# Performance work log

Measured on AMD Instinct MI355X. Metric: run time of the kernel, lower is better.

## Reference

```python
import jax, jax.numpy as jnp
import numpy as np


def sobel_kernels_3d(dtype=jnp.float32):
    # Standard 3D Sobel: derivative [-1,0,1] along one axis, smoothing [1,2,1]
    # along the other two. Returns shape (3, 1, 3, 3, 3) in OIDHW layout.
    s = jnp.array([1.0, 2.0, 1.0], dtype=dtype)
    d = jnp.array([-1.0, 0.0, 1.0], dtype=dtype)
    kd = jnp.einsum('i,j,k->ijk', d, s, s)  # d/dD
    kh = jnp.einsum('i,j,k->ijk', s, d, s)  # d/dH
    kw = jnp.einsum('i,j,k->ijk', s, s, d)  # d/dW
    return jnp.stack([kd, kh, kw], axis=0)[:, None]  # (3,1,3,3,3)


def _grad3d(x, kernels):
    # x: (B, C, D, H, W) -> flatten (B*C, 1, D, H, W), conv with padding=1.
    B, C, D, H, W = x.shape
    x_ = x.reshape(B * C, 1, D, H, W)
    return jax.lax.conv_general_dilated(
        x_, kernels.astype(x.dtype),
        window_strides=(1, 1, 1),
        padding=((1, 1), (1, 1), (1, 1)),
        dimension_numbers=('NCDHW', 'OIDHW', 'NCDHW'),
    )  # (B*C, 3, D, H, W)


def setup_inputs() -> dict:
    key = jax.random.key(0)
    k1, k2 = jax.random.split(key)
    shape = (4, 4, 64, 128, 128)
    pred = jax.random.normal(k1, shape, dtype=jnp.float32)
    target = jax.random.normal(k2, shape, dtype=jnp.float32)
    return {"pred": pred, "target": target}


def reference(pred, target):
    kernels = sobel_kernels_3d(pred.dtype)
    grad_pred = _grad3d(pred, kernels)
    grad_target = _grad3d(target, kernels)
    # loss_type == 'l1'
    return jnp.mean(jnp.abs(grad_pred - grad_target))
```

## Files before the change

kernel.cpp:

```cpp
#include <hip/hip_runtime.h>

#define NB 16
#define DD 64
#define HH 128
#define WW 128
#define HW (HH * WW)

constexpr int CD = 2;
constexpr int TH = 8;
constexpr int LZ = CD + 2;
constexpr int LY = TH + 2;
constexpr int PL = LY * WW;
constexpr int NPOS = LZ * LY * (WW / 4);
constexpr int SLOTS = NPOS / 256;
constexpr int NT = 8;
constexpr int NQ = 4;
constexpr float INV_COUNT = 1.0f / 50331648.0f;

__global__ void zero_out_kernel(float* out) {
    if (threadIdx.x == 0 && blockIdx.x == 0) out[0] = 0.0f;
}

__global__ __launch_bounds__(256) void sobel_l1_kernel(
    const float* __restrict__ pred,
    const float* __restrict__ target,
    float* __restrict__ out)
{
    __shared__ float t[2][LZ * PL];

    const int tid = threadIdx.x;
    int b = blockIdx.x;
    const int bh   = b & 15; b >>= 4;
    const int q    = b & 3;  b >>= 2;
    const int bn   = b;

    const int h0 = bh * TH;
    const int dbase = q * (NT * CD);
    const size_t nbase = (size_t)bn * (size_t)(DD * HW);

    int  soff[SLOTS];
    int  sz[SLOTS];
    bool sokh[SLOTS];
#pragma unroll
    for (int k = 0; k < SLOTS; ++k) {
        const int i  = k * 256 + tid;
        const int q4 = i & 31;
        const int ry = i >> 5;
        const int z  = ry / LY;
        const int y  = ry - z * LY;
        const int gh = h0 - 1 + y;
        sokh[k] = (unsigned)gh < HH;
        soff[k] = min(max(gh, 0), HH - 1) * WW + 4 * q4;
        sz[k]   = z;
    }

    float4 sp[SLOTS], sq[SLOTS];

    auto load_tile = [&](int tau) {
        const int d0 = dbase + tau * CD;
#pragma unroll
        for (int k = 0; k < SLOTS; ++k) {
            const int gd  = d0 - 1 + sz[k];
            const int gdc = min(max(gd, 0), DD - 1);
            const size_t idx = nbase + (size_t)gdc * HW + soff[k];
            sp[k] = *(const float4*)(pred + idx);
            sq[k] = *(const float4*)(target + idx);
        }
    };

    auto store_tile = [&](int tau, float* B) {
        const int d0 = dbase + tau * CD;
#pragma unroll
        for (int k = 0; k < SLOTS; ++k) {
            const int gd = d0 - 1 + sz[k];
            const float m = (sokh[k] && (unsigned)gd < DD) ? 1.0f : 0.0f;
            const int i = k * 256 + tid;
            const float4 v = float4{(sp[k].x - sq[k].x) * m,
                                    (sp[k].y - sq[k].y) * m,
                                    (sp[k].z - sq[k].z) * m,
                                    (sp[k].w - sq[k].w) * m};
            *(float4*)&B[4 * i] = v;
        }
    };

    const int tc = tid & 31;
    const int lh = tid >> 5;

    auto compute_tile = [&](const float* B, float& acc) {
        auto plane_l = [&](int z, float4& A_, float4& Bh_, float4& Bw_) {
            float4 rs[3], rdw[3];
#pragma unroll
            for (int r = 0; r < 3; ++r) {
                const float4 v = *(const float4*)&B[z * PL + (lh + r) * WW + 4 * tc];
                float lm = __shfl_up(v.w, 1, 32);
                float rp = __shfl_down(v.x, 1, 32);
                if (tc == 0)  lm = 0.f;
                if (tc == 31) rp = 0.f;
                rs[r]  = float4{lm  + 2.f * v.x + v.y,
                                v.x + 2.f * v.y + v.z,
                                v.y + 2.f * v.z + v.w,
                                v.z + 2.f * v.w + rp};
                rdw[r] = float4{v.y - lm, v.z - v.x, v.w - v.y, rp - v.z};
            }
            A_  = float4{rs[0].x + 2.f * rs[1].x + rs[2].x,
                         rs[0].y + 2.f * rs[1].y + rs[2].y,
                         rs[0].z + 2.f * rs[1].z + rs[2].z,
                         rs[0].w + 2.f * rs[1].w + rs[2].w};
            Bh_ = float4{rs[2].x - rs[0].x, rs[2].y - rs[0].y,
                         rs[2].z - rs[0].z, rs[2].w - rs[0].w};
            Bw_ = float4{rdw[0].x + 2.f * rdw[1].x + rdw[2].x,
                         rdw[0].y + 2.f * rdw[1].y + rdw[2].y,
                         rdw[0].z + 2.f * rdw[1].z + rdw[2].z,
                         rdw[0].w + 2.f * rdw[1].w + rdw[2].w};
        };

        float4 rA[3], rBh[3], rBw[3];
        plane_l(0, rA[0], rBh[0], rBw[0]);
        plane_l(1, rA[1], rBh[1], rBw[1]);
#pragma unroll
        for (int ld = 0; ld < CD; ++ld) {
            const int s0 = ld % 3, s1 = (ld + 1) % 3, s2 = (ld + 2) % 3;
            plane_l(ld + 2, rA[s2], rBh[s2], rBw[s2]);
            const float4 a0 = rA[s0],  a2 = rA[s2];
            const float4 b0 = rBh[s0], b1 = rBh[s1], b2 = rBh[s2];
            const float4 c0 = rBw[s0], c1 = rBw[s1], c2 = rBw[s2];
            acc += fabsf(a2.x - a0.x) + fabsf(a2.y - a0.y)
                 + fabsf(a2.z - a0.z) + fabsf(a2.w - a0.w);
            acc += fabsf(b0.x + 2.f * b1.x + b2.x) + fabsf(b0.y + 2.f * b1.y + b2.y)
                 + fabsf(b0.z + 2.f * b1.z + b2.z) + fabsf(b0.w + 2.f * b1.w + b2.w);
            acc += fabsf(c0.x + 2.f * c1.x + c2.x) + fabsf(c0.y + 2.f * c1.y + c2.y)
                 + fabsf(c0.z + 2.f * c1.z + c2.z) + fabsf(c0.w + 2.f * c1.w + c2.w);
        }
    };

    float acc = 0.0f;
    load_tile(0);
    store_tile(0, t[0]);
    __syncthreads();
    for (int tau = 0; tau < NT; ++tau) {
        if (tau + 1 < NT) load_tile(tau + 1);
        compute_tile(t[tau & 1], acc);
        if (tau + 1 < NT) store_tile(tau + 1, t[(tau + 1) & 1]);
        __syncthreads();
    }

#pragma unroll
    for (int off = 32; off > 0; off >>= 1)
        acc += __shfl_down(acc, off, 64);
    if ((tid & 63) == 0) t[0][tid >> 6] = acc;
    __syncthreads();
    if (tid == 0) {
        const float s = t[0][0] + t[0][1] + t[0][2] + t[0][3];
        atomicAdd(out, s * INV_COUNT);
    }
}

extern "C" void kernel_launch(void* const* d_in, const int* in_sizes, int n_in,
                              void* d_out, int out_size, void* d_ws, size_t ws_size,
                              hipStream_t stream) {
    const float* pred   = (const float*)d_in[0];
    const float* target = (const float*)d_in[1];
    float* out = (float*)d_out;

    zero_out_kernel<<<1, 64, 0, stream>>>(out);

    const int nblocks = NB * NQ * (HH / TH);
    sobel_l1_kernel<<<nblocks, 256, 0, stream>>>(pred, target, out);
}
```

Before: 155.4 us.

## Replace double-buffered depth tiles with a six-plane LDS ring buffer

Each depth step previously loaded four planes from global memory into a fresh shared-memory buffer, re-reading the two halo planes the previous step already held. This version keeps a six-plane ring in shared memory and fetches only the two new planes per step, with the remaining 128-thread slot handling the plane remainder. The goal is to roughly halve global read traffic and cut LDS usage, which, together with a launch-bounds occupancy hint, could allow more resident blocks. The cost is extra indexing and ring-slot arithmetic, plus an uneven load split across threads.

```diff
diff --git a/kernel.cpp b/kernel.cpp
--- a/kernel.cpp
+++ b/kernel.cpp
@@ -6,92 +6,96 @@
 #define WW 128
 #define HW (HH * WW)
 
-constexpr int CD = 2;
 constexpr int TH = 8;
-constexpr int LZ = CD + 2;
 constexpr int LY = TH + 2;
 constexpr int PL = LY * WW;
-constexpr int NPOS = LZ * LY * (WW / 4);
-constexpr int SLOTS = NPOS / 256;
+constexpr int RING = 6;
 constexpr int NT = 8;
 constexpr int NQ = 4;
+constexpr int SLOTS = 3;
 constexpr float INV_COUNT = 1.0f / 50331648.0f;
 
 __global__ void zero_out_kernel(float* out) {
     if (threadIdx.x == 0 && blockIdx.x == 0) out[0] = 0.0f;
 }
 
-__global__ __launch_bounds__(256) void sobel_l1_kernel(
+__global__ __launch_bounds__(256, 4) void sobel_l1_kernel(
     const float* __restrict__ pred,
     const float* __restrict__ target,
     float* __restrict__ out)
 {
-    __shared__ float t[2][LZ * PL];
+    __shared__ float ring[RING * PL];
 
     const int tid = threadIdx.x;
     int b = blockIdx.x;
-    const int bh   = b & 15; b >>= 4;
-    const int q    = b & 3;  b >>= 2;
-    const int bn   = b;
+    const int bh = b & 15; b >>= 4;
+    const int q  = b & 3;  b >>= 2;
+    const int bn = b;
 
     const int h0 = bh * TH;
-    const int dbase = q * (NT * CD);
+    const int dbase = q * (NT * 2);
     const size_t nbase = (size_t)bn * (size_t)(DD * HW);
 
+    const bool k2ok = tid < 128;
     int  soff[SLOTS];
+    int  stoff[SLOTS];
     int  sz[SLOTS];
     bool sokh[SLOTS];
 #pragma unroll
     for (int k = 0; k < SLOTS; ++k) {
-        const int i  = k * 256 + tid;
-        const int q4 = i & 31;
-        const int ry = i >> 5;
-        const int z  = ry / LY;
-        const int y  = ry - z * LY;
+        const int i  = (k < 2) ? (k * 256 + tid) : (512 + (tid & 127));
+        const int z  = i / 320;
+        const int r  = i - z * 320;
+        const int y  = r >> 5;
+        const int q4 = r & 31;
         const int gh = h0 - 1 + y;
-        sokh[k] = (unsigned)gh < HH;
-        soff[k] = min(max(gh, 0), HH - 1) * WW + 4 * q4;
-        sz[k]   = z;
+        sokh[k]  = (unsigned)gh < HH;
+        soff[k]  = min(max(gh, 0), HH - 1) * WW + 4 * q4;
+        stoff[k] = y * WW + 4 * q4;
+        sz[k]    = z;
     }
 
     float4 sp[SLOTS], sq[SLOTS];
 
-    auto load_tile = [&](int tau) {
-        const int d0 = dbase + tau * CD;
+    auto load_pair = [&](int p0) {
 #pragma unroll
         for (int k = 0; k < SLOTS; ++k) {
-            const int gd  = d0 - 1 + sz[k];
-            const int gdc = min(max(gd, 0), DD - 1);
-            const size_t idx = nbase + (size_t)gdc * HW + soff[k];
-            sp[k] = *(const float4*)(pred + idx);
-            sq[k] = *(const float4*)(target + idx);
+            if (k < 2 || k2ok) {
+                const int gd  = dbase + p0 + sz[k];
+                const int gdc = min(max(gd, 0), DD - 1);
+                const size_t idx = nbase + (size_t)gdc * HW + soff[k];
+                sp[k] = *(const float4*)(pred + idx);
+                sq[k] = *(const float4*)(target + idx);
+            }
         }
     };
 
-    auto store_tile = [&](int tau, float* B) {
-        const int d0 = dbase + tau * CD;
+    auto store_pair = [&](int p0) {
+        const int base0 = ((p0 + 1) % RING) * PL;
+        const int base1 = ((p0 + 2) % RING) * PL;
 #pragma unroll
         for (int k = 0; k < SLOTS; ++k) {
-            const int gd = d0 - 1 + sz[k];
-            const float m = (sokh[k] && (unsigned)gd < DD) ? 1.0f : 0.0f;
-            const int i = k * 256 + tid;
-            const float4 v = float4{(sp[k].x - sq[k].x) * m,
-                                    (sp[k].y - sq[k].y) * m,
-                                    (sp[k].z - sq[k].z) * m,
-                                    (sp[k].w - sq[k].w) * m};
-            *(float4*)&B[4 * i] = v;
+            if (k < 2 || k2ok) {
+                const int gd = dbase + p0 + sz[k];
+                const float m = (sokh[k] && (unsigned)gd < DD) ? 1.0f : 0.0f;
+                float* dst = &ring[(sz[k] ? base1 : base0) + stoff[k]];
+                *(float4*)dst = float4{(sp[k].x - sq[k].x) * m,
+                                       (sp[k].y - sq[k].y) * m,
+                                       (sp[k].z - sq[k].z) * m,
+                                       (sp[k].w - sq[k].w) * m};
+            }
         }
     };
 
     const int tc = tid & 31;
     const int lh = tid >> 5;
 
-    auto compute_tile = [&](const float* B, float& acc) {
-        auto plane_l = [&](int z, float4& A_, float4& Bh_, float4& Bw_) {
+    auto compute_tile = [&](int tau, float& acc) {
+        auto plane_l = [&](int base, float4& A_, float4& Bh_, float4& Bw_) {
             float4 rs[3], rdw[3];
 #pragma unroll
             for (int r = 0; r < 3; ++r) {
-                const float4 v = *(const float4*)&B[z * PL + (lh + r) * WW + 4 * tc];
+                const float4 v = *(const float4*)&ring[base + (lh + r) * WW + 4 * tc];
                 float lm = __shfl_up(v.w, 1, 32);
                 float rp = __shfl_down(v.x, 1, 32);
                 if (tc == 0)  lm = 0.f;
@@ -114,13 +118,17 @@
                          rdw[0].w + 2.f * rdw[1].w + rdw[2].w};
         };
 
+        int sb[4];
+#pragma unroll
+        for (int j = 0; j < 4; ++j) sb[j] = ((2 * tau + j) % RING) * PL;
+
         float4 rA[3], rBh[3], rBw[3];
-        plane_l(0, rA[0], rBh[0], rBw[0]);
-        plane_l(1, rA[1], rBh[1], rBw[1]);
+        plane_l(sb[0], rA[0], rBh[0], rBw[0]);
+        plane_l(sb[1], rA[1], rBh[1], rBw[1]);
 #pragma unroll
-        for (int ld = 0; ld < CD; ++ld) {
+        for (int ld = 0; ld < 2; ++ld) {
             const int s0 = ld % 3, s1 = (ld + 1) % 3, s2 = (ld + 2) % 3;
-            plane_l(ld + 2, rA[s2], rBh[s2], rBw[s2]);
+            plane_l(sb[ld + 2], rA[s2], rBh[s2], rBw[s2]);
             const float4 a0 = rA[s0],  a2 = rA[s2];
             const float4 b0 = rBh[s0], b1 = rBh[s1], b2 = rBh[s2];
             const float4 c0 = rBw[s0], c1 = rBw[s1], c2 = rBw[s2];
@@ -133,24 +141,25 @@
         }
     };
 
+    load_pair(-1); store_pair(-1);
+    load_pair(1);  store_pair(1);
+    __syncthreads();
+
     float acc = 0.0f;
-    load_tile(0);
-    store_tile(0, t[0]);
-    __syncthreads();
     for (int tau = 0; tau < NT; ++tau) {
-        if (tau + 1 < NT) load_tile(tau + 1);
-        compute_tile(t[tau & 1], acc);
-        if (tau + 1 < NT) store_tile(tau + 1, t[(tau + 1) & 1]);
+        if (tau + 1 < NT) load_pair(2 * tau + 3);
+        compute_tile(tau, acc);
+        if (tau + 1 < NT) store_pair(2 * tau + 3);
         __syncthreads();
     }
 
 #pragma unroll
     for (int off = 32; off > 0; off >>= 1)
         acc += __shfl_down(acc, off, 64);
-    if ((tid & 63) == 0) t[0][tid >> 6] = acc;
+    if ((tid & 63) == 0) ring[tid >> 6] = acc;
     __syncthreads();
     if (tid == 0) {
-        const float s = t[0][0] + t[0][1] + t[0][2] + t[0][3];
+        const float s = ring[0] + ring[1] + ring[2] + ring[3];
         atomicAdd(out, s * INV_COUNT);
     }
 }
```

Result: no change. 156.5 us (+0.7%).
